# Optimization experiments

Hardware: AMD Instinct MI355X
Metric: run time of the kernel (lower is better)

The kernel has to match this reference:

```python
import jax, jax.numpy as jnp
import numpy as np

NUM_CLASSES = 2
THRESH = 0.5        # overlap_thresh
NEGPOS = 3          # neg:pos ratio
VAR = (0.1, 0.2)    # cfg['variance']
B, P, O = 64, 32768, 50


def point_form(p):
    # center-size [cx,cy,w,h] -> corner [xmin,ymin,xmax,ymax]
    return jnp.concatenate([p[:, :2] - p[:, 2:] * 0.5, p[:, :2] + p[:, 2:] * 0.5], axis=1)


def iou(a, b):
    # a [O,4], b [P,4] corner form -> [O,P]
    lt = jnp.maximum(a[:, None, :2], b[None, :, :2])
    rb = jnp.minimum(a[:, None, 2:], b[None, :, 2:])
    wh = jnp.clip(rb - lt, 0.0, None)
    inter = wh[..., 0] * wh[..., 1]
    area_a = ((a[:, 2] - a[:, 0]) * (a[:, 3] - a[:, 1]))[:, None]
    area_b = ((b[:, 2] - b[:, 0]) * (b[:, 3] - b[:, 1]))[None, :]
    return inter / (area_a + area_b - inter)


def encode(matched, priors_cs):
    g_cxcy = ((matched[:, :2] + matched[:, 2:]) * 0.5 - priors_cs[:, :2]) / (VAR[0] * priors_cs[:, 2:])
    g_wh = jnp.log((matched[:, 2:] - matched[:, :2]) / priors_cs[:, 2:]) / VAR[1]
    return jnp.concatenate([g_cxcy, g_wh], axis=1)


def match_one(truths, labels, priors_cs, priors_pt):
    ovl = iou(truths, priors_pt)                # [O,P]
    best_prior_idx = jnp.argmax(ovl, axis=1)    # [O] best prior per GT
    best_truth_ovl = jnp.max(ovl, axis=0)       # [P]
    best_truth_idx = jnp.argmax(ovl, axis=0)    # [P]
    best_truth_ovl = best_truth_ovl.at[best_prior_idx].set(2.0)
    best_truth_idx = best_truth_idx.at[best_prior_idx].set(jnp.arange(truths.shape[0]))
    matched = truths[best_truth_idx]            # [P,4]
    conf = jnp.where(best_truth_ovl < THRESH, 0, labels[best_truth_idx])
    return encode(matched, priors_cs), conf


def reference(arm_loc, arm_conf, odm_loc, odm_conf, priors, targets):
    loc_data, conf_data = arm_loc, arm_conf    # use_ARM=False -> ARM branch
    num, num_priors = loc_data.shape[0], loc_data.shape[1]
    truths = targets[..., :4]
    labels = (targets[..., 4] >= 0).astype(jnp.int32)   # num_classes == 2 binarization
    priors_pt = point_form(priors)
    loc_t, conf_t = jax.vmap(lambda t, l: match_one(t, l, priors, priors_pt))(truths, labels)
    loc_t = jax.lax.stop_gradient(loc_t)
    conf_t = jax.lax.stop_gradient(conf_t)
    pos = conf_t > 0                             # [B,P]
    # localization: smooth L1, summed over positives
    d = loc_data - loc_t
    ad = jnp.abs(d)
    sl1 = jnp.where(ad < 1.0, 0.5 * d * d, ad - 0.5)
    loss_l = jnp.sum(sl1 * pos[..., None].astype(loc_data.dtype))
    # per-prior conf loss for hard negative mining
    lse = jax.nn.logsumexp(conf_data, axis=-1)   # [B,P]
    picked = jnp.take_along_axis(conf_data, conf_t[..., None], axis=-1)[..., 0]
    lc = lse - picked                            # NLL per prior
    lc_mine = jnp.where(pos, 0.0, lc)            # zero positives before ranking
    order = jnp.argsort(-lc_mine, axis=1)        # descending sort
    rank = jnp.argsort(order, axis=1)            # rank of each prior
    num_pos = jnp.sum(pos, axis=1, keepdims=True)            # [B,1]
    num_neg = jnp.minimum(NEGPOS * num_pos, num_priors - 1)
    neg = rank < num_neg
    sel = (pos | neg).astype(conf_data.dtype)
    loss_c = jnp.sum(lc * sel)
    N = jnp.sum(num_pos).astype(loc_data.dtype)
    return loss_l / N, loss_c / N


def setup_inputs():
    key = jax.random.key(0)
    ks = jax.random.split(key, 8)
    arm_loc = jax.random.normal(ks[0], (B, P, 4), jnp.float32)
    arm_conf = jax.random.normal(ks[1], (B, P, NUM_CLASSES), jnp.float32)
    odm_loc = jax.random.normal(ks[2], (B, P, 4), jnp.float32)
    odm_conf = jax.random.normal(ks[3], (B, P, NUM_CLASSES), jnp.float32)
    # priors in center-size form
    p_cxcy = jax.random.uniform(ks[4], (P, 2), jnp.float32, 0.05, 0.95)
    p_wh = jax.random.uniform(ks[5], (P, 2), jnp.float32, 0.05, 0.5)
    priors = jnp.concatenate([p_cxcy, p_wh], axis=1)
    # GT boxes in corner form with valid extents, labels >= 0
    t_cxcy = jax.random.uniform(ks[6], (B, O, 2), jnp.float32, 0.2, 0.8)
    t_wh = jax.random.uniform(ks[7], (B, O, 2), jnp.float32, 0.05, 0.3)
    boxes = jnp.concatenate([t_cxcy - t_wh * 0.5, t_cxcy + t_wh * 0.5], axis=-1)
    targets = jnp.concatenate([boxes, jnp.ones((B, O, 1), jnp.float32)], axis=-1)
    return {"arm_loc": arm_loc, "arm_conf": arm_conf, "odm_loc": odm_loc,
            "odm_conf": odm_conf, "priors": priors, "targets": targets}
```

## Files before the change

### kernel.cpp

```cpp
#include <hip/hip_runtime.h>
#include <cstdint>

#pragma clang fp contract(off)

#define BB 64
#define PP 32768
#define OO 50
#define THRESH_F 0.5f
#define VAR0 0.1f
#define VAR1 0.2f
#define NEGPOS_I 3
#define SS 32
#define T1 4
#define NB_P0 256
#define NB_P1 4096
#define NB_P2 2048
#define NCELL 1024

typedef unsigned long long u64;

__device__ __forceinline__ unsigned mpart4(unsigned x) {
    x = (x | (x << 2)) & 0x33u;
    x = (x | (x << 1)) & 0x55u;
    return x;
}
__device__ __forceinline__ int cell_of(float4 pr) {
    int xb = (int)(pr.x * 16.0f); xb = xb < 0 ? 0 : (xb > 15 ? 15 : xb);
    int yb = (int)(pr.y * 16.0f); yb = yb < 0 ? 0 : (yb > 15 ? 15 : yb);
    float s = fmaxf(pr.z, pr.w);
    int wc = s < 0.275f ? 0 : (s < 0.368f ? 1 : (s < 0.44f ? 2 : 3));
    return wc * 256 + (int)(mpart4((unsigned)xb) | (mpart4((unsigned)yb) << 1));
}

__global__ void k_zero(float4* __restrict__ dst, int n4) {
    int i = blockIdx.x * blockDim.x + threadIdx.x;
    if (i < n4) dst[i] = make_float4(0.f, 0.f, 0.f, 0.f);
}

__global__ void __launch_bounds__(1024)
k_prep(const float4* __restrict__ pri, int* __restrict__ perm, int* __restrict__ iperm) {
    __shared__ int cnt[NCELL];
    __shared__ int tmp[NCELL];
    int tid = threadIdx.x;
    cnt[tid] = 0;
    __syncthreads();
    for (int i = 0; i < 32; ++i)
        atomicAdd(&cnt[cell_of(pri[i * 1024 + tid])], 1);
    __syncthreads();
    int v = cnt[tid]; tmp[tid] = v;
    __syncthreads();
    for (int off = 1; off < 1024; off <<= 1) {
        int a = (tid >= off) ? tmp[tid - off] : 0;
        __syncthreads(); tmp[tid] += a; __syncthreads();
    }
    cnt[tid] = tmp[tid] - v;
    __syncthreads();
    for (int i = 0; i < 32; ++i) {
        int p = i * 1024 + tid;
        int c = cell_of(pri[p]);
        int pos = atomicAdd(&cnt[c], 1);
        perm[pos] = p;
        iperm[p] = pos;
    }
}

#define DPP_MAX(x, ctrl, rmask)                                              \
    {                                                                        \
        int _o = __float_as_int(x);                                          \
        x = fmaxf(x, __int_as_float(__builtin_amdgcn_update_dpp(             \
                _o, _o, (ctrl), (rmask), 0xf, false)));                      \
    }
#define DPP_MINF(x, ctrl, rmask)                                             \
    {                                                                        \
        int _o = __float_as_int(x);                                          \
        x = fminf(x, __int_as_float(__builtin_amdgcn_update_dpp(             \
                _o, _o, (ctrl), (rmask), 0xf, false)));                      \
    }
#define WAVE_MAXF(x) { DPP_MAX(x,0x111,0xf); DPP_MAX(x,0x112,0xf); DPP_MAX(x,0x114,0xf); \
                       DPP_MAX(x,0x118,0xf); DPP_MAX(x,0x142,0xa); DPP_MAX(x,0x143,0xc); }
#define WAVE_MINF(x) { DPP_MINF(x,0x111,0xf); DPP_MINF(x,0x112,0xf); DPP_MINF(x,0x114,0xf); \
                       DPP_MINF(x,0x118,0xf); DPP_MINF(x,0x142,0xa); DPP_MINF(x,0x143,0xc); }

__device__ __forceinline__ float sl1enc(const float* __restrict__ tb,
                                        float4 pr, float4 ld) {
    float gx = ((tb[0] + tb[2]) * 0.5f - pr.x) / (VAR0 * pr.z);
    float gy = ((tb[1] + tb[3]) * 0.5f - pr.y) / (VAR0 * pr.w);
    float gw = logf((tb[2] - tb[0]) / pr.z) / VAR1;
    float gh = logf((tb[3] - tb[1]) / pr.w) / VAR1;
    float g[4] = {gx, gy, gw, gh};
    float l[4] = {ld.x, ld.y, ld.z, ld.w};
    float s = 0.f;
    for (int q = 0; q < 4; ++q) {
        float d = l[q] - g[q];
        float ad = fabsf(d);
        s += (ad < 1.0f) ? 0.5f * d * d : ad - 0.5f;
    }
    return s;
}

__global__ void __launch_bounds__(256, 8)
k_ml(const float* __restrict__ priors, const int* __restrict__ perm,
     const float* __restrict__ targets,
     const float* __restrict__ arm_loc, const float* __restrict__ arm_conf,
     float* __restrict__ lcmP, unsigned char* __restrict__ bpiP,
     u64* __restrict__ bpm,
     float* __restrict__ pll, float* __restrict__ pplc, int* __restrict__ pnp,
     int* __restrict__ Hc0, float* __restrict__ Hs0) {
    __shared__ float4 trP[OO];
    __shared__ float2 trQ[OO];
    __shared__ int   hc[NB_P0];
    __shared__ float hs[NB_P0];
    __shared__ float s1[256]; __shared__ float s2[256]; __shared__ int s3[256];
    int b = (blockIdx.x % 8) * 8 + (blockIdx.y % 8);
    int s = (blockIdx.x / 8) + 4 * (blockIdx.y / 8);
    int tid = threadIdx.x;
    if (tid < OO) {
        const float* tb = &targets[(size_t)(b * OO + tid) * 5];
        float x0 = tb[0], y0 = tb[1], x1 = tb[2], y1 = tb[3];
        trP[tid] = make_float4(x0, y0, x1, y1);
        trQ[tid] = make_float2((x1 - x0) * (y1 - y0), tb[4]);
    }
    hc[tid] = 0; hs[tid] = 0.f;
    __syncthreads();

    int p0 = s * (256 * T1) + tid * T1;
    int4 o4 = ((const int4*)perm)[p0 >> 2];
    int o_[T1] = {o4.x, o4.y, o4.z, o4.w};
    int omin = min(min(o_[0], o_[1]), min(o_[2], o_[3]));
    float bx0[T1], by0[T1], bx1[T1], by1[T1], aB[T1];
#pragma unroll
    for (int j = 0; j < T1; ++j) {
        float4 pr = ((const float4*)priors)[o_[j]];
        bx0[j] = pr.x - pr.z * 0.5f; by0[j] = pr.y - pr.w * 0.5f;
        bx1[j] = pr.x + pr.z * 0.5f; by1[j] = pr.y + pr.w * 0.5f;
        aB[j] = (bx1[j] - bx0[j]) * (by1[j] - by0[j]);
    }
    float lx0 = fminf(fminf(bx0[0], bx0[1]), fminf(bx0[2], bx0[3]));
    float ly0 = fminf(fminf(by0[0], by0[1]), fminf(by0[2], by0[3]));
    float lx1 = fmaxf(fmaxf(bx1[0], bx1[1]), fmaxf(bx1[2], bx1[3]));
    float ly1 = fmaxf(fmaxf(by1[0], by1[1]), fmaxf(by1[2], by1[3]));
    WAVE_MINF(lx0); WAVE_MINF(ly0); WAVE_MAXF(lx1); WAVE_MAXF(ly1);
    float wx0 = __int_as_float(__builtin_amdgcn_readlane(__float_as_int(lx0), 63));
    float wy0 = __int_as_float(__builtin_amdgcn_readlane(__float_as_int(ly0), 63));
    float wx1 = __int_as_float(__builtin_amdgcn_readlane(__float_as_int(lx1), 63));
    float wy1 = __int_as_float(__builtin_amdgcn_readlane(__float_as_int(ly1), 63));

    float rbv[T1]; int rbi[T1];
#pragma unroll
    for (int j = 0; j < T1; ++j) { rbv[j] = 0.0f; rbi[j] = 0; }

    for (int t = 0; t < OO; ++t) {
        float4 tP = trP[t];
        if (!(tP.z > wx0 && tP.x < wx1 && tP.w > wy0 && tP.y < wy1)) continue;
        float aA = trQ[t].x;
        float I[T1];
#pragma unroll
        for (int j = 0; j < T1; ++j) {
            float ltx = fmaxf(tP.x, bx0[j]), lty = fmaxf(tP.y, by0[j]);
            float rbx = fminf(tP.z, bx1[j]), rby = fminf(tP.w, by1[j]);
            float wx = fmaxf(rbx - ltx, 0.f), wy = fmaxf(rby - lty, 0.f);
            I[j] = wx * wy;
        }
        bool anyl = (I[0] > 0.f) | (I[1] > 0.f) | (I[2] > 0.f) | (I[3] > 0.f);
        if (__any(anyl)) {
            float cbv = 0.0f; int cbo = omin;
#pragma unroll
            for (int j = 0; j < T1; ++j) {
                float v = I[j] / (aA + aB[j] - I[j]);
                if (v > rbv[j]) { rbv[j] = v; rbi[j] = t; }
                if (v > cbv || (v == cbv && o_[j] < cbo)) { cbv = v; cbo = o_[j]; }
            }
            float x = cbv;
            WAVE_MAXF(x);
            float mvf = __int_as_float(__builtin_amdgcn_readlane(__float_as_int(x), 63));
            if (mvf > 0.0f) {
                u64 msk = __ballot(cbv == mvf);
                int ln = (int)__ffsll((long long)msk) - 1;
                int morig = __builtin_amdgcn_readlane(cbo, ln);
                u64 rest = msk & (msk - 1);
                while (rest) {
                    int l2 = (int)__ffsll((long long)rest) - 1;
                    int o2 = __builtin_amdgcn_readlane(cbo, l2);
                    morig = min(morig, o2);
                    rest &= rest - 1;
                }
                if ((tid & 63) == 0) {
                    u64 pk = ((u64)__float_as_uint(mvf) << 32) | (unsigned)(PP - morig);
                    atomicMax(&bpm[b * OO + t], pk);
                }
            }
        }
    }

    size_t bbase = (size_t)b * PP;
    float ll = 0.0f, plc = 0.0f; int np = 0;
    float outv[4]; unsigned pbyte = 0;
#pragma unroll
    for (int c = 0; c < T1; ++c) {
        int o = o_[c]; size_t bo = bbase + o;
        int ti = rbi[c]; float ov = rbv[c];
        float2 cf = ((const float2*)arm_conf)[bo];
        float c0 = cf.x, c1 = cf.y;
        float m = fmaxf(c0, c1);
        float lse = logf(expf(c0 - m) + expf(c1 - m)) + m;
        bool pos = (ov >= THRESH_F) && (trQ[ti].y >= 0.0f);
        float lc = lse - (pos ? c1 : c0);
        outv[c] = pos ? 0.0f : lc;
        pbyte |= (unsigned)((pos ? 0x80u : 0u) | (unsigned)ti) << (8 * c);
        unsigned u = __float_as_uint(outv[c]);
        atomicAdd(&hc[u >> 23], 1);
        atomicAdd(&hs[u >> 23], outv[c]);
        if (pos) {
            np++; plc += lc;
            float4 pr = ((const float4*)priors)[o];
            float4 ld = ((const float4*)arm_loc)[bo];
            const float4 tv = trP[ti];
            float tb4[4] = {tv.x, tv.y, tv.z, tv.w};
            ll += sl1enc(tb4, pr, ld);
        }
    }
    size_t bq = bbase + p0;
    ((float4*)lcmP)[bq >> 2] = make_float4(outv[0], outv[1], outv[2], outv[3]);
    ((unsigned*)bpiP)[bq >> 2] = pbyte;

    __syncthreads();
    {
        int cv = hc[tid];
        if (cv) {
            atomicAdd(&Hc0[b * NB_P0 + tid], cv);
            atomicAdd(&Hs0[b * NB_P0 + tid], hs[tid]);
        }
    }
    s1[tid] = ll; s2[tid] = plc; s3[tid] = np;
    __syncthreads();
    for (int st = 128; st > 0; st >>= 1) {
        if (tid < st) { s1[tid] += s1[tid+st]; s2[tid] += s2[tid+st]; s3[tid] += s3[tid+st]; }
        __syncthreads();
    }
    if (tid == 0) {
        pll[s * BB + b] = s1[0];
        pplc[s * BB + b] = s2[0];
        pnp[s * BB + b] = s3[0];
    }
}

__global__ void k_fix(const u64* __restrict__ bpm, const float* __restrict__ targets,
                      const float* __restrict__ arm_loc, const float* __restrict__ arm_conf,
                      const float* __restrict__ priors, const int* __restrict__ iperm,
                      const unsigned char* __restrict__ bpiP, float* __restrict__ lcmP,
                      float* __restrict__ pll, float* __restrict__ pplc,
                      int* __restrict__ pnp, int* __restrict__ npb,
                      int* __restrict__ Hc0, float* __restrict__ Hs0) {
    int b = blockIdx.x, j = threadIdx.x;
    int p = -1;
    if (j < OO) {
        unsigned lo = (unsigned)(bpm[b * OO + j] & 0xFFFFFFFFull);
        p = lo ? (PP - (int)lo) : 0;
    }
    bool w = (j < OO);
    for (int jj = 1; jj < OO; ++jj) {
        int pj = __shfl(p, jj, 64);
        if (jj > j && pj == p) w = false;
    }
    float dll = 0.f, dplc = 0.f; int dnp = 0;
    if (w) {
        int pos_ = iperm[p];
        size_t bq = (size_t)b * PP + pos_;
        size_t bo = (size_t)b * PP + p;
        unsigned char ob = bpiP[bq];
        bool old_pos = (ob & 0x80u) != 0;
        int old_ti = ob & 63;
        float2 cf = ((const float2*)arm_conf)[bo];
        float c0 = cf.x, c1 = cf.y;
        float m = fmaxf(c0, c1);
        float lse = logf(expf(c0 - m) + expf(c1 - m)) + m;
        const float* tbj = &targets[(size_t)(b * OO + j) * 5];
        bool new_pos = (tbj[4] >= 0.0f);
        float old_lcm = lcmP[bq];
        float new_lcm = new_pos ? 0.0f : (lse - c0);
        unsigned uo = __float_as_uint(old_lcm), un = __float_as_uint(new_lcm);
        if (uo != un) {
            atomicAdd(&Hc0[b * NB_P0 + (uo >> 23)], -1);
            atomicAdd(&Hs0[b * NB_P0 + (uo >> 23)], -old_lcm);
            atomicAdd(&Hc0[b * NB_P0 + (un >> 23)], 1);
            atomicAdd(&Hs0[b * NB_P0 + (un >> 23)], new_lcm);
            lcmP[bq] = new_lcm;
        }
        float4 pr = ((const float4*)priors)[p];
        float4 ld = ((const float4*)arm_loc)[bo];
        if (old_pos) {
            dnp -= 1; dplc -= (lse - c1);
            dll -= sl1enc(&targets[(size_t)(b * OO + old_ti) * 5], pr, ld);
        }
        if (new_pos) {
            dnp += 1; dplc += (lse - c1);
            dll += sl1enc(tbj, pr, ld);
        }
    }
    int myp = (j < SS) ? pnp[j * BB + b] : 0;
    for (int st = 32; st >= 1; st >>= 1) {
        dll += __shfl_down(dll, st, 64);
        dplc += __shfl_down(dplc, st, 64);
        dnp += __shfl_down(dnp, st, 64);
        myp += __shfl_down(myp, st, 64);
    }
    if (j == 0) {
        pll[b] += dll;
        pplc[b] += dplc;
        pnp[b] += dnp;
        npb[b] = myp + dnp;
    }
}

__global__ void __launch_bounds__(256)
k_sel(const float* __restrict__ lcmP, const int* __restrict__ npb,
      const int* __restrict__ Hc0, const float* __restrict__ Hs0,
      float* __restrict__ ssum, int* __restrict__ srem, unsigned* __restrict__ stb) {
    __shared__ int hc[NB_P1]; __shared__ float hs[NB_P1];
    __shared__ int sc[256]; __shared__ float sf[256];
    __shared__ int s_chunk, s_r; __shared__ float s_S; __shared__ unsigned s_pref;
    int b = blockIdx.x, tid = threadIdx.x;
    const float4* v4 = (const float4*)(lcmP + (size_t)b * PP);

    {
        int c = Hc0[b * NB_P0 + tid];
        float f = Hs0[b * NB_P0 + tid];
        sc[tid] = c; sf[tid] = f;
        if (tid == 0) {
            int k = NEGPOS_I * npb[b]; if (k > PP - 1) k = PP - 1;
            s_r = k; s_S = 0.f;
        }
        __syncthreads();
        for (int off = 1; off < 256; off <<= 1) {
            int cv = (tid + off < 256) ? sc[tid + off] : 0;
            float fv = (tid + off < 256) ? sf[tid + off] : 0.f;
            __syncthreads(); sc[tid] += cv; sf[tid] += fv; __syncthreads();
        }
        int r = s_r;
        int nxt = (tid == 255) ? 0 : sc[tid + 1];
        if (sc[tid] >= r && nxt < r) s_chunk = tid;
        __syncthreads();
        if (tid == 0) {
            int ch = s_chunk;
            s_pref = (unsigned)ch;
            s_r = r - ((ch == 255) ? 0 : sc[ch + 1]);
            s_S = (ch == 255) ? 0.f : sf[ch + 1];
        }
        __syncthreads();
    }
    {
        for (int i = tid; i < NB_P1; i += 256) { hc[i] = 0; hs[i] = 0.f; }
        __syncthreads();
        unsigned pref = s_pref;
        for (int it = 0; it < 32; ++it) {
            float4 x = v4[it * 256 + tid];
            float xs[4] = {x.x, x.y, x.z, x.w};
            for (int c2 = 0; c2 < 4; ++c2) {
                unsigned u = __float_as_uint(xs[c2]);
                if ((u >> 23) == pref) {
                    atomicAdd(&hc[(u >> 11) & 4095u], 1);
                    atomicAdd(&hs[(u >> 11) & 4095u], xs[c2]);
                }
            }
        }
        __syncthreads();
        int c = 0; float f = 0.f; int base = tid * 16;
        for (int i = 0; i < 16; ++i) { c += hc[base + i]; f += hs[base + i]; }
        sc[tid] = c; sf[tid] = f; __syncthreads();
        for (int off = 1; off < 256; off <<= 1) {
            int cv = (tid + off < 256) ? sc[tid + off] : 0;
            float fv = (tid + off < 256) ? sf[tid + off] : 0.f;
            __syncthreads(); sc[tid] += cv; sf[tid] += fv; __syncthreads();
        }
        int r = s_r;
        int nxt = (tid == 255) ? 0 : sc[tid + 1];
        if (sc[tid] >= r && nxt < r) s_chunk = tid;
        __syncthreads();
        if (tid == 0) {
            int ch = s_chunk;
            int r2 = r - ((ch == 255) ? 0 : sc[ch + 1]);
            float S2 = s_S + ((ch == 255) ? 0.f : sf[ch + 1]);
            int binSel = ch * 16;
            for (int i = 15; i >= 0; --i) {
                int bin = ch * 16 + i; int cbn = hc[bin];
                if (r2 <= cbn) { binSel = bin; break; }
                r2 -= cbn; S2 += hs[bin];
            }
            s_pref = (s_pref << 12) | (unsigned)binSel; s_r = r2; s_S = S2;
        }
        __syncthreads();
    }
    {
        for (int i = tid; i < NB_P2; i += 256) { hc[i] = 0; hs[i] = 0.f; }
        __syncthreads();
        unsigned pref = s_pref;
        for (int it = 0; it < 32; ++it) {
            float4 x = v4[it * 256 + tid];
            float xs[4] = {x.x, x.y, x.z, x.w};
            for (int c2 = 0; c2 < 4; ++c2) {
                unsigned u = __float_as_uint(xs[c2]);
                if ((u >> 11) == pref) {
                    atomicAdd(&hc[u & 2047u], 1);
                    atomicAdd(&hs[u & 2047u], xs[c2]);
                }
            }
        }
        __syncthreads();
        int c = 0; float f = 0.f; int base = tid * 8;
        for (int i = 0; i < 8; ++i) { c += hc[base + i]; f += hs[base + i]; }
        sc[tid] = c; sf[tid] = f; __syncthreads();
        for (int off = 1; off < 256; off <<= 1) {
            int cv = (tid + off < 256) ? sc[tid + off] : 0;
            float fv = (tid + off < 256) ? sf[tid + off] : 0.f;
            __syncthreads(); sc[tid] += cv; sf[tid] += fv; __syncthreads();
        }
        int r = s_r;
        int nxt = (tid == 255) ? 0 : sc[tid + 1];
        if (sc[tid] >= r && nxt < r) s_chunk = tid;
        __syncthreads();
        if (tid == 0) {
            int ch = s_chunk;
            int r2 = r - ((ch == 255) ? 0 : sc[ch + 1]);
            float S2 = s_S + ((ch == 255) ? 0.f : sf[ch + 1]);
            int binSel = ch * 8;
            for (int i = 7; i >= 0; --i) {
                int bin = ch * 8 + i; int cbn = hc[bin];
                if (r2 <= cbn) { binSel = bin; break; }
                r2 -= cbn; S2 += hs[bin];
            }
            stb[b] = (s_pref << 11) | (unsigned)binSel;
            srem[b] = r2; ssum[b] = S2;
        }
    }
}

__global__ void k_final(const float* __restrict__ pll, const float* __restrict__ pplc,
                        const int* __restrict__ pnp, const float* __restrict__ ssum,
                        const int* __restrict__ srem, const unsigned* __restrict__ stb,
                        float* __restrict__ out) {
    int b = threadIdx.x;
    float ll = 0.f, plc = 0.f; int np = 0;
    for (int s = 0; s < SS; ++s) {
        ll += pll[s * BB + b];
        plc += pplc[s * BB + b];
        np += pnp[s * BB + b];
    }
    float tval = __uint_as_float(stb[b]);
    float cc = plc + ssum[b] + (float)srem[b] * tval;
    for (int s = 32; s > 0; s >>= 1) {
        ll += __shfl_down(ll, s);
        cc += __shfl_down(cc, s);
        np += __shfl_down(np, s);
    }
    if (b == 0) {
        float N = (float)np;
        out[0] = ll / N;
        out[1] = cc / N;
    }
}

extern "C" void kernel_launch(void* const* d_in, const int* in_sizes, int n_in,
                              void* d_out, int out_size, void* d_ws, size_t ws_size,
                              hipStream_t stream) {
    const float* arm_loc  = (const float*)d_in[0];
    const float* arm_conf = (const float*)d_in[1];
    const float* priors   = (const float*)d_in[4];
    const float* targets  = (const float*)d_in[5];
    float* out = (float*)d_out;

    char* w = (char*)d_ws;
    float* lcmP = (float*)w;  w += sizeof(float) * (size_t)BB * PP;
    unsigned char* bpiP = (unsigned char*)w; w += (size_t)BB * PP;
    char* zbase = w;
    int*   Hc0 = (int*)w;    w += sizeof(int)   * BB * NB_P0;
    float* Hs0 = (float*)w;  w += sizeof(float) * BB * NB_P0;
    u64*   bpm = (u64*)w;    w += sizeof(u64)   * BB * OO;
    size_t zbytes = (size_t)(w - zbase);
    int*   perm  = (int*)w;  w += sizeof(int) * PP;
    int*   iperm = (int*)w;  w += sizeof(int) * PP;
    float* pll  = (float*)w; w += sizeof(float) * BB * SS;
    float* pplc = (float*)w; w += sizeof(float) * BB * SS;
    int*   pnp  = (int*)w;   w += sizeof(int)   * BB * SS;
    int*   npb  = (int*)w;   w += sizeof(int)   * BB;
    int*      srem = (int*)w;      w += sizeof(int) * BB;
    float*    ssum = (float*)w;    w += sizeof(float) * BB;
    unsigned* stb  = (unsigned*)w; w += sizeof(unsigned) * BB;

    int n4 = (int)(zbytes / 16);
    k_zero<<<(n4 + 255) / 256, 256, 0, stream>>>((float4*)zbase, n4);
    k_prep<<<1, 1024, 0, stream>>>((const float4*)priors, perm, iperm);
    k_ml<<<dim3(SS, BB), 256, 0, stream>>>(priors, perm, targets, arm_loc, arm_conf,
                                           lcmP, bpiP, bpm, pll, pplc, pnp, Hc0, Hs0);
    k_fix<<<BB, 64, 0, stream>>>(bpm, targets, arm_loc, arm_conf, priors, iperm,
                                 bpiP, lcmP, pll, pplc, pnp, npb, Hc0, Hs0);
    k_sel<<<BB, 256, 0, stream>>>(lcmP, npb, Hc0, Hs0, ssum, srem, stb);
    k_final<<<1, 64, 0, stream>>>(pll, pplc, pnp, ssum, srem, stb, out);
}
```

Before: 289.6 us.

## Parallelize prior binning across blocks and privatize per-wave LDS histograms

The single-block prior sorting kernel becomes two multi-block kernels: a global-atomic cell histogram, then a per-block prefix scan with global cursors that scatters perm/iperm. This removes a serial 1024-thread single-CU stage. The per-block loss histogram in k_ml is split into four per-wave copies to cut LDS atomic contention, and the copies are summed before the global flush. The cost is one extra launch, more global atomics, and a perm order within each cell that is no longer deterministic.

```diff
diff --git a/kernel.cpp b/kernel.cpp
--- a/kernel.cpp
+++ b/kernel.cpp
@@ -37,30 +37,34 @@
     if (i < n4) dst[i] = make_float4(0.f, 0.f, 0.f, 0.f);
 }
 
-__global__ void __launch_bounds__(1024)
-k_prep(const float4* __restrict__ pri, int* __restrict__ perm, int* __restrict__ iperm) {
-    __shared__ int cnt[NCELL];
-    __shared__ int tmp[NCELL];
+__global__ void k_phist(const float4* __restrict__ pri, int* __restrict__ cnt) {
+    int p = blockIdx.x * 1024 + threadIdx.x * 4;
+    for (int j = 0; j < 4; ++j)
+        atomicAdd(&cnt[cell_of(pri[p + j])], 1);
+}
+
+__global__ void __launch_bounds__(256)
+k_pss(const float4* __restrict__ pri, const int* __restrict__ cnt,
+      int* __restrict__ cursor, int* __restrict__ perm, int* __restrict__ iperm) {
+    __shared__ int sc[256];
+    __shared__ int sbase[NCELL];
     int tid = threadIdx.x;
-    cnt[tid] = 0;
+    int a[4]; int s = 0;
+    for (int i = 0; i < 4; ++i) { a[i] = cnt[tid * 4 + i]; s += a[i]; }
+    sc[tid] = s; __syncthreads();
+    for (int off = 1; off < 256; off <<= 1) {
+        int v = (tid >= off) ? sc[tid - off] : 0;
+        __syncthreads(); sc[tid] += v; __syncthreads();
+    }
+    int excl = sc[tid] - s;
+    for (int i = 0; i < 4; ++i) { sbase[tid * 4 + i] = excl; excl += a[i]; }
     __syncthreads();
-    for (int i = 0; i < 32; ++i)
-        atomicAdd(&cnt[cell_of(pri[i * 1024 + tid])], 1);
-    __syncthreads();
-    int v = cnt[tid]; tmp[tid] = v;
-    __syncthreads();
-    for (int off = 1; off < 1024; off <<= 1) {
-        int a = (tid >= off) ? tmp[tid - off] : 0;
-        __syncthreads(); tmp[tid] += a; __syncthreads();
-    }
-    cnt[tid] = tmp[tid] - v;
-    __syncthreads();
-    for (int i = 0; i < 32; ++i) {
-        int p = i * 1024 + tid;
-        int c = cell_of(pri[p]);
-        int pos = atomicAdd(&cnt[c], 1);
-        perm[pos] = p;
-        iperm[p] = pos;
+    int p = blockIdx.x * 1024 + tid * 4;
+    for (int j = 0; j < 4; ++j) {
+        int c = cell_of(pri[p + j]);
+        int pos = sbase[c] + atomicAdd(&cursor[c], 1);
+        perm[pos] = p + j;
+        iperm[p + j] = pos;
     }
 }
 
@@ -108,8 +112,8 @@
      int* __restrict__ Hc0, float* __restrict__ Hs0) {
     __shared__ float4 trP[OO];
     __shared__ float2 trQ[OO];
-    __shared__ int   hc[NB_P0];
-    __shared__ float hs[NB_P0];
+    __shared__ int   hc[4 * NB_P0];
+    __shared__ float hs[4 * NB_P0];
     __shared__ float s1[256]; __shared__ float s2[256]; __shared__ int s3[256];
     int b = (blockIdx.x % 8) * 8 + (blockIdx.y % 8);
     int s = (blockIdx.x / 8) + 4 * (blockIdx.y / 8);
@@ -120,7 +124,7 @@
         trP[tid] = make_float4(x0, y0, x1, y1);
         trQ[tid] = make_float2((x1 - x0) * (y1 - y0), tb[4]);
     }
-    hc[tid] = 0; hs[tid] = 0.f;
+    for (int i = tid; i < 4 * NB_P0; i += 256) { hc[i] = 0; hs[i] = 0.f; }
     __syncthreads();
 
     int p0 = s * (256 * T1) + tid * T1;
@@ -193,6 +197,7 @@
     }
 
     size_t bbase = (size_t)b * PP;
+    int hb = (tid >> 6) * NB_P0;
     float ll = 0.0f, plc = 0.0f; int np = 0;
     float outv[4]; unsigned pbyte = 0;
 #pragma unroll
@@ -208,8 +213,8 @@
         outv[c] = pos ? 0.0f : lc;
         pbyte |= (unsigned)((pos ? 0x80u : 0u) | (unsigned)ti) << (8 * c);
         unsigned u = __float_as_uint(outv[c]);
-        atomicAdd(&hc[u >> 23], 1);
-        atomicAdd(&hs[u >> 23], outv[c]);
+        atomicAdd(&hc[hb + (u >> 23)], 1);
+        atomicAdd(&hs[hb + (u >> 23)], outv[c]);
         if (pos) {
             np++; plc += lc;
             float4 pr = ((const float4*)priors)[o];
@@ -225,10 +230,11 @@
 
     __syncthreads();
     {
-        int cv = hc[tid];
+        int cv = hc[tid] + hc[NB_P0 + tid] + hc[2*NB_P0 + tid] + hc[3*NB_P0 + tid];
         if (cv) {
+            float sv = hs[tid] + hs[NB_P0 + tid] + hs[2*NB_P0 + tid] + hs[3*NB_P0 + tid];
             atomicAdd(&Hc0[b * NB_P0 + tid], cv);
-            atomicAdd(&Hs0[b * NB_P0 + tid], hs[tid]);
+            atomicAdd(&Hs0[b * NB_P0 + tid], sv);
         }
     }
     s1[tid] = ll; s2[tid] = plc; s3[tid] = np;
@@ -475,6 +481,8 @@
     int*   Hc0 = (int*)w;    w += sizeof(int)   * BB * NB_P0;
     float* Hs0 = (float*)w;  w += sizeof(float) * BB * NB_P0;
     u64*   bpm = (u64*)w;    w += sizeof(u64)   * BB * OO;
+    int*   cellCnt = (int*)w; w += sizeof(int) * NCELL;
+    int*   cursor  = (int*)w; w += sizeof(int) * NCELL;
     size_t zbytes = (size_t)(w - zbase);
     int*   perm  = (int*)w;  w += sizeof(int) * PP;
     int*   iperm = (int*)w;  w += sizeof(int) * PP;
@@ -488,7 +496,8 @@
 
     int n4 = (int)(zbytes / 16);
     k_zero<<<(n4 + 255) / 256, 256, 0, stream>>>((float4*)zbase, n4);
-    k_prep<<<1, 1024, 0, stream>>>((const float4*)priors, perm, iperm);
+    k_phist<<<PP / 1024, 256, 0, stream>>>((const float4*)priors, cellCnt);
+    k_pss<<<PP / 1024, 256, 0, stream>>>((const float4*)priors, cellCnt, cursor, perm, iperm);
     k_ml<<<dim3(SS, BB), 256, 0, stream>>>(priors, perm, targets, arm_loc, arm_conf,
                                            lcmP, bpiP, bpm, pll, pplc, pnp, Hc0, Hs0);
     k_fix<<<BB, 64, 0, stream>>>(bpm, targets, arm_loc, arm_conf, priors, iperm,
```

Result: faster. 265.0 us (-8.5%).

## Parallelize prior binning, fuse zeroing and final reduction, privatize LDS histograms

Applied to the files above, without the earlier changes.

The single-block prior counting sort becomes 32 blocks. Each block recomputes the global cell counts plus its own prefix offsets, and also zeroes the workspace, so k_zero is gone. k_fix now folds the per-slice partial sums into per-batch totals. k_sel finishes the whole loss with global atomics and a last-block-done counter, so k_final is dropped. k_ml gives each wavefront its own shared-memory histogram to cut atomic contention. Together this removes two kernel launches and the serial prep block, at the cost of redundant counting work in every prep block and float atomic reductions whose summation order is nondeterministic.

```diff
diff --git a/kernel.cpp b/kernel.cpp
--- a/kernel.cpp
+++ b/kernel.cpp
@@ -16,6 +16,7 @@
 #define NB_P1 4096
 #define NB_P2 2048
 #define NCELL 1024
+#define PREPB 32
 
 typedef unsigned long long u64;
 
@@ -32,31 +33,38 @@
     return wc * 256 + (int)(mpart4((unsigned)xb) | (mpart4((unsigned)yb) << 1));
 }
 
-__global__ void k_zero(float4* __restrict__ dst, int n4) {
-    int i = blockIdx.x * blockDim.x + threadIdx.x;
-    if (i < n4) dst[i] = make_float4(0.f, 0.f, 0.f, 0.f);
-}
-
-__global__ void __launch_bounds__(1024)
-k_prep(const float4* __restrict__ pri, int* __restrict__ perm, int* __restrict__ iperm) {
+__global__ void __launch_bounds__(512)
+k_prep(const float4* __restrict__ pri, int* __restrict__ perm, int* __restrict__ iperm,
+       float4* __restrict__ zdst, int zn4) {
     __shared__ int cnt[NCELL];
-    __shared__ int tmp[NCELL];
-    int tid = threadIdx.x;
-    cnt[tid] = 0;
+    __shared__ int pref[NCELL];
+    __shared__ int scn[512];
+    int tid = threadIdx.x, blk = blockIdx.x;
+    for (int i = blk * 512 + tid; i < zn4; i += PREPB * 512)
+        zdst[i] = make_float4(0.f, 0.f, 0.f, 0.f);
+    cnt[tid] = 0; cnt[tid + 512] = 0;
+    pref[tid] = 0; pref[tid + 512] = 0;
     __syncthreads();
-    for (int i = 0; i < 32; ++i)
-        atomicAdd(&cnt[cell_of(pri[i * 1024 + tid])], 1);
+    int pstart = blk * (PP / PREPB);
+    for (int p = tid; p < PP; p += 512) {
+        int c = cell_of(pri[p]);
+        atomicAdd(&cnt[c], 1);
+        if (p < pstart) atomicAdd(&pref[c], 1);
+    }
     __syncthreads();
-    int v = cnt[tid]; tmp[tid] = v;
+    int a0 = cnt[2 * tid], a1 = cnt[2 * tid + 1];
+    int s = a0 + a1;
+    scn[tid] = s; __syncthreads();
+    for (int off = 1; off < 512; off <<= 1) {
+        int v = (tid >= off) ? scn[tid - off] : 0;
+        __syncthreads(); scn[tid] += v; __syncthreads();
+    }
+    int excl = scn[tid] - s;
+    cnt[2 * tid]     = excl + pref[2 * tid];
+    cnt[2 * tid + 1] = excl + a0 + pref[2 * tid + 1];
     __syncthreads();
-    for (int off = 1; off < 1024; off <<= 1) {
-        int a = (tid >= off) ? tmp[tid - off] : 0;
-        __syncthreads(); tmp[tid] += a; __syncthreads();
-    }
-    cnt[tid] = tmp[tid] - v;
-    __syncthreads();
-    for (int i = 0; i < 32; ++i) {
-        int p = i * 1024 + tid;
+    for (int k = 0; k < 2; ++k) {
+        int p = pstart + tid * 2 + k;
         int c = cell_of(pri[p]);
         int pos = atomicAdd(&cnt[c], 1);
         perm[pos] = p;
@@ -108,8 +116,8 @@
      int* __restrict__ Hc0, float* __restrict__ Hs0) {
     __shared__ float4 trP[OO];
     __shared__ float2 trQ[OO];
-    __shared__ int   hc[NB_P0];
-    __shared__ float hs[NB_P0];
+    __shared__ int   hc[4 * NB_P0];
+    __shared__ float hs[4 * NB_P0];
     __shared__ float s1[256]; __shared__ float s2[256]; __shared__ int s3[256];
     int b = (blockIdx.x % 8) * 8 + (blockIdx.y % 8);
     int s = (blockIdx.x / 8) + 4 * (blockIdx.y / 8);
@@ -120,7 +128,7 @@
         trP[tid] = make_float4(x0, y0, x1, y1);
         trQ[tid] = make_float2((x1 - x0) * (y1 - y0), tb[4]);
     }
-    hc[tid] = 0; hs[tid] = 0.f;
+    for (int i = tid; i < 4 * NB_P0; i += 256) { hc[i] = 0; hs[i] = 0.f; }
     __syncthreads();
 
     int p0 = s * (256 * T1) + tid * T1;
@@ -193,6 +201,7 @@
     }
 
     size_t bbase = (size_t)b * PP;
+    int hb = (tid >> 6) * NB_P0;
     float ll = 0.0f, plc = 0.0f; int np = 0;
     float outv[4]; unsigned pbyte = 0;
 #pragma unroll
@@ -208,8 +217,8 @@
         outv[c] = pos ? 0.0f : lc;
         pbyte |= (unsigned)((pos ? 0x80u : 0u) | (unsigned)ti) << (8 * c);
         unsigned u = __float_as_uint(outv[c]);
-        atomicAdd(&hc[u >> 23], 1);
-        atomicAdd(&hs[u >> 23], outv[c]);
+        atomicAdd(&hc[hb + (u >> 23)], 1);
+        atomicAdd(&hs[hb + (u >> 23)], outv[c]);
         if (pos) {
             np++; plc += lc;
             float4 pr = ((const float4*)priors)[o];
@@ -225,10 +234,11 @@
 
     __syncthreads();
     {
-        int cv = hc[tid];
+        int cv = hc[tid] + hc[NB_P0 + tid] + hc[2*NB_P0 + tid] + hc[3*NB_P0 + tid];
         if (cv) {
+            float sv = hs[tid] + hs[NB_P0 + tid] + hs[2*NB_P0 + tid] + hs[3*NB_P0 + tid];
             atomicAdd(&Hc0[b * NB_P0 + tid], cv);
-            atomicAdd(&Hs0[b * NB_P0 + tid], hs[tid]);
+            atomicAdd(&Hs0[b * NB_P0 + tid], sv);
         }
     }
     s1[tid] = ll; s2[tid] = plc; s3[tid] = np;
@@ -248,8 +258,10 @@
                       const float* __restrict__ arm_loc, const float* __restrict__ arm_conf,
                       const float* __restrict__ priors, const int* __restrict__ iperm,
                       const unsigned char* __restrict__ bpiP, float* __restrict__ lcmP,
-                      float* __restrict__ pll, float* __restrict__ pplc,
-                      int* __restrict__ pnp, int* __restrict__ npb,
+                      const float* __restrict__ pll, const float* __restrict__ pplc,
+                      const int* __restrict__ pnp,
+                      float* __restrict__ llb, float* __restrict__ plcb,
+                      int* __restrict__ npb,
                       int* __restrict__ Hc0, float* __restrict__ Hs0) {
     int b = blockIdx.x, j = threadIdx.x;
     int p = -1;
@@ -297,25 +309,29 @@
             dll += sl1enc(tbj, pr, ld);
         }
     }
-    int myp = (j < SS) ? pnp[j * BB + b] : 0;
+    float myll = (j < SS) ? pll[j * BB + b] : 0.f;
+    float mypl = (j < SS) ? pplc[j * BB + b] : 0.f;
+    int   mynp = (j < SS) ? pnp[j * BB + b] : 0;
+    dll += myll; dplc += mypl; dnp += mynp;
     for (int st = 32; st >= 1; st >>= 1) {
         dll += __shfl_down(dll, st, 64);
         dplc += __shfl_down(dplc, st, 64);
         dnp += __shfl_down(dnp, st, 64);
-        myp += __shfl_down(myp, st, 64);
     }
     if (j == 0) {
-        pll[b] += dll;
-        pplc[b] += dplc;
-        pnp[b] += dnp;
-        npb[b] = myp + dnp;
+        llb[b] = dll;
+        plcb[b] = dplc;
+        npb[b] = dnp;
     }
 }
 
 __global__ void __launch_bounds__(256)
-k_sel(const float* __restrict__ lcmP, const int* __restrict__ npb,
+k_sel(const float* __restrict__ lcmP,
+      const float* __restrict__ llb, const float* __restrict__ plcb,
+      const int* __restrict__ npb,
       const int* __restrict__ Hc0, const float* __restrict__ Hs0,
-      float* __restrict__ ssum, int* __restrict__ srem, unsigned* __restrict__ stb) {
+      float* __restrict__ gacc, int* __restrict__ gcnt,
+      float* __restrict__ out) {
     __shared__ int hc[NB_P1]; __shared__ float hs[NB_P1];
     __shared__ int sc[256]; __shared__ float sf[256];
     __shared__ int s_chunk, s_r; __shared__ float s_S; __shared__ unsigned s_pref;
@@ -428,34 +444,25 @@
                 if (r2 <= cbn) { binSel = bin; break; }
                 r2 -= cbn; S2 += hs[bin];
             }
-            stb[b] = (s_pref << 11) | (unsigned)binSel;
-            srem[b] = r2; ssum[b] = S2;
-        }
-    }
-}
-
-__global__ void k_final(const float* __restrict__ pll, const float* __restrict__ pplc,
-                        const int* __restrict__ pnp, const float* __restrict__ ssum,
-                        const int* __restrict__ srem, const unsigned* __restrict__ stb,
-                        float* __restrict__ out) {
-    int b = threadIdx.x;
-    float ll = 0.f, plc = 0.f; int np = 0;
-    for (int s = 0; s < SS; ++s) {
-        ll += pll[s * BB + b];
-        plc += pplc[s * BB + b];
-        np += pnp[s * BB + b];
-    }
-    float tval = __uint_as_float(stb[b]);
-    float cc = plc + ssum[b] + (float)srem[b] * tval;
-    for (int s = 32; s > 0; s >>= 1) {
-        ll += __shfl_down(ll, s);
-        cc += __shfl_down(cc, s);
-        np += __shfl_down(np, s);
-    }
-    if (b == 0) {
-        float N = (float)np;
-        out[0] = ll / N;
-        out[1] = cc / N;
+            unsigned tb = (s_pref << 11) | (unsigned)binSel;
+            float tval = __uint_as_float(tb);
+            float ccb = plcb[b] + S2 + (float)r2 * tval;
+            float llv = llb[b]; int npv = npb[b];
+            atomicAdd(&gacc[0], llv);
+            atomicAdd(&gacc[1], ccb);
+            atomicAdd(&gcnt[0], npv);
+            __threadfence();
+            int tk = atomicAdd(&gcnt[1], 1);
+            if (tk == BB - 1) {
+                __threadfence();
+                float llt = atomicAdd(&gacc[0], 0.f);
+                float cct = atomicAdd(&gacc[1], 0.f);
+                int npt = atomicAdd(&gcnt[0], 0);
+                float N = (float)npt;
+                out[0] = llt / N;
+                out[1] = cct / N;
+            }
+        }
     }
 }
 
@@ -475,24 +482,24 @@
     int*   Hc0 = (int*)w;    w += sizeof(int)   * BB * NB_P0;
     float* Hs0 = (float*)w;  w += sizeof(float) * BB * NB_P0;
     u64*   bpm = (u64*)w;    w += sizeof(u64)   * BB * OO;
+    float* gacc = (float*)w; w += sizeof(float) * 2;
+    int*   gcnt = (int*)w;   w += sizeof(int)   * 2;
     size_t zbytes = (size_t)(w - zbase);
     int*   perm  = (int*)w;  w += sizeof(int) * PP;
     int*   iperm = (int*)w;  w += sizeof(int) * PP;
     float* pll  = (float*)w; w += sizeof(float) * BB * SS;
     float* pplc = (float*)w; w += sizeof(float) * BB * SS;
     int*   pnp  = (int*)w;   w += sizeof(int)   * BB * SS;
+    float* llb  = (float*)w; w += sizeof(float) * BB;
+    float* plcb = (float*)w; w += sizeof(float) * BB;
     int*   npb  = (int*)w;   w += sizeof(int)   * BB;
-    int*      srem = (int*)w;      w += sizeof(int) * BB;
-    float*    ssum = (float*)w;    w += sizeof(float) * BB;
-    unsigned* stb  = (unsigned*)w; w += sizeof(unsigned) * BB;
-
-    int n4 = (int)(zbytes / 16);
-    k_zero<<<(n4 + 255) / 256, 256, 0, stream>>>((float4*)zbase, n4);
-    k_prep<<<1, 1024, 0, stream>>>((const float4*)priors, perm, iperm);
+
+    int zn4 = (int)(zbytes / 16);
+    k_prep<<<PREPB, 512, 0, stream>>>((const float4*)priors, perm, iperm,
+                                      (float4*)zbase, zn4);
     k_ml<<<dim3(SS, BB), 256, 0, stream>>>(priors, perm, targets, arm_loc, arm_conf,
                                            lcmP, bpiP, bpm, pll, pplc, pnp, Hc0, Hs0);
     k_fix<<<BB, 64, 0, stream>>>(bpm, targets, arm_loc, arm_conf, priors, iperm,
-                                 bpiP, lcmP, pll, pplc, pnp, npb, Hc0, Hs0);
-    k_sel<<<BB, 256, 0, stream>>>(lcmP, npb, Hc0, Hs0, ssum, srem, stb);
-    k_final<<<1, 64, 0, stream>>>(pll, pplc, pnp, ssum, srem, stb, out);
-}
+                                 bpiP, lcmP, pll, pplc, pnp, llb, plcb, npb, Hc0, Hs0);
+    k_sel<<<BB, 256, 0, stream>>>(lcmP, llb, plcb, npb, Hc0, Hs0, gacc, gcnt, out);
+}
```

After: 271.9 us. 6.1% less time.
